# Kernel optimization log

Hardware: AMD Instinct MI355X
Metric: run time of the kernel (lower is better)

## Reference

```python
import jax, jax.numpy as jnp
import numpy as np

EMBED_DIM = 2048
NUM_HEADS = 16
HEAD_DIM = EMBED_DIM // NUM_HEADS
BASE = 10000.0


def rotate_half(x):
    half = x.shape[-1] // 2
    x1, x2 = x[..., :half], x[..., half:]
    return jnp.concatenate([-x2, x1], axis=-1)


def apply_rope(x, base=BASE):
    # x: [B, H, S, Dh]
    S, Dh = x.shape[-2], x.shape[-1]
    inv_freq = 1.0 / (base ** (jnp.arange(0, Dh, 2, dtype=jnp.float32) / Dh))
    t = jnp.arange(S, dtype=jnp.float32)
    freqs = jnp.einsum('i,j->ij', t, inv_freq)          # [S, Dh/2]
    emb = jnp.concatenate([freqs, freqs], axis=-1)      # [S, Dh]
    return x * jnp.cos(emb) + rotate_half(x) * jnp.sin(emb)


def setup_inputs() -> dict:
    key = jax.random.key(0)
    ks = jax.random.split(key, 9)
    B, S, D = 2, 2048, EMBED_DIM
    xavier = lambda k, shape: jax.random.uniform(
        k, shape, jnp.float32, -1.0, 1.0) * float(np.sqrt(6.0 / (shape[0] + shape[1])))
    return {
        'x': jax.random.normal(ks[0], (B, S, D), jnp.float32),
        'q_w': xavier(ks[1], (D, D)),
        'k_w': xavier(ks[2], (D, D)),
        'v_w': xavier(ks[3], (D, D)),
        'q_b': jnp.zeros((D,), jnp.float32),
        'k_b': jnp.zeros((D,), jnp.float32),
        'v_b': jnp.zeros((D,), jnp.float32),
        'out_w': xavier(ks[4], (D, D)),
        'out_b': jnp.zeros((D,), jnp.float32),
    }


def reference(x, q_w, k_w, v_w, q_b, k_b, v_b, out_w, out_b):
    B, S, D = x.shape
    H, Dh = NUM_HEADS, HEAD_DIM
    scaling = Dh ** -0.5
    # F.linear(x, W, b) = x @ W.T + b
    q = (x @ q_w.T + q_b).reshape(B, S, H, Dh).transpose(0, 2, 1, 3)
    k = (x @ k_w.T + k_b).reshape(B, S, H, Dh).transpose(0, 2, 1, 3)
    v = (x @ v_w.T + v_b).reshape(B, S, H, Dh).transpose(0, 2, 1, 3)
    q = apply_rope(q)
    k = apply_rope(k)
    attn = jnp.einsum('bhqd,bhkd->bhqk', q, k) * scaling
    probs = jax.nn.softmax(attn, axis=-1)
    out = jnp.einsum('bhqk,bhkd->bhqd', probs, v)
    out = out.transpose(0, 2, 1, 3).reshape(B, S, D)
    return out @ out_w.T + out_b
```

## Files before the change

### kernel.cpp

```cpp
#include <hip/hip_runtime.h>
#include <stdint.h>

typedef __bf16 bf16;
typedef __bf16 bf16x4 __attribute__((ext_vector_type(4)));
typedef __bf16 bf16x8 __attribute__((ext_vector_type(8)));
typedef float f32x4 __attribute__((ext_vector_type(4)));

#define DM 2048
#define MM 4096
#define MFMA16(a, b, c) __builtin_amdgcn_mfma_f32_16x16x32_bf16(a, b, c, 0, 0, 0)

__device__ __forceinline__ void gload_lds16(const void* g, void* l) {
  __builtin_amdgcn_global_load_lds((const __attribute__((address_space(1))) uint32_t*)g,
                                   (__attribute__((address_space(3))) uint32_t*)l, 16, 0, 0);
}

__global__ __launch_bounds__(256) void cvt_f32_bf16(
    const float* __restrict__ s0, const float* __restrict__ s1,
    const float* __restrict__ s2, const float* __restrict__ s3,
    const float* __restrict__ s4,
    bf16* __restrict__ d0, bf16* __restrict__ d1, bf16* __restrict__ d2,
    bf16* __restrict__ d3, bf16* __restrict__ d4)
{
  const size_t i4 = (size_t)(blockIdx.x * 256 + threadIdx.x) * 4;
  const float* s; bf16* d; size_t off;
  if      (i4 <  8388608u) { s = s0; d = d0; off = i4;             }
  else if (i4 < 12582912u) { s = s1; d = d1; off = i4 -  8388608u; }
  else if (i4 < 16777216u) { s = s2; d = d2; off = i4 - 12582912u; }
  else if (i4 < 20971520u) { s = s3; d = d3; off = i4 - 16777216u; }
  else                     { s = s4; d = d4; off = i4 - 20971520u; }
  const float4 v = *(const float4*)(s + off);
  bf16x4 o = { (bf16)v.x, (bf16)v.y, (bf16)v.z, (bf16)v.w };
  *(bf16x4*)(d + off) = o;
}

__global__ __launch_bounds__(256) void gemm_qkv(
    const bf16* __restrict__ A,
    const bf16* __restrict__ Wq, const bf16* __restrict__ Wk, const bf16* __restrict__ Wv,
    const float* __restrict__ qb, const float* __restrict__ kb, const float* __restrict__ vb,
    bf16* __restrict__ Cq, bf16* __restrict__ Ck, bf16* __restrict__ Cv)
{
  const int bz = blockIdx.z;
  const bf16*  W    = (bz == 0) ? Wq : (bz == 1) ? Wk : Wv;
  const float* bias = (bz == 0) ? qb : (bz == 1) ? kb : vb;

  __shared__ __align__(16) bf16 As[128 * 32];
  __shared__ __align__(16) bf16 Bs[128 * 32];
  const int t = threadIdx.x;
  const int wave = t >> 6, lane = t & 63;
  const int quad = lane >> 4, c16 = lane & 15;
  const int wr = wave >> 1, wc = wave & 1;
  const int m0 = blockIdx.y * 128, n0 = blockIdx.x * 128;

  f32x4 acc[4][4] = {};

  const int rowA = t >> 2;
  const int colA = (t & 3) * 8;
  const bf16* gA = A + (size_t)(m0 + rowA) * DM + colA;
  const bf16* gB = W + (size_t)(n0 + rowA) * DM + colA;
  bf16* lA = As + wave * 512;
  bf16* lB = Bs + wave * 512;

  for (int k0 = 0; k0 < DM; k0 += 32) {
    gload_lds16(gA, lA);
    gload_lds16(gA + (size_t)64 * DM, lA + 2048);
    gload_lds16(gB, lB);
    gload_lds16(gB + (size_t)64 * DM, lB + 2048);
    gA += 32; gB += 32;
    __syncthreads();

    bf16x8 af[4], bfr[4];
#pragma unroll
    for (int i = 0; i < 4; ++i)
      af[i] = *(const bf16x8*)&As[(wr * 64 + i * 16 + c16) * 32 + quad * 8];
#pragma unroll
    for (int j = 0; j < 4; ++j)
      bfr[j] = *(const bf16x8*)&Bs[(wc * 64 + j * 16 + c16) * 32 + quad * 8];
#pragma unroll
    for (int i = 0; i < 4; ++i)
#pragma unroll
      for (int j = 0; j < 4; ++j)
        acc[i][j] = MFMA16(af[i], bfr[j], acc[i][j]);
    __syncthreads();
  }

  if (bz != 2) {
    bf16* C = (bz == 0) ? Cq : Ck;
#pragma unroll
    for (int j = 0; j < 4; ++j) {
      const int col = n0 + wc * 64 + j * 16 + c16;
      const float bv = bias[col];
#pragma unroll
      for (int i = 0; i < 4; ++i) {
        const int row = m0 + wr * 64 + i * 16 + quad * 4;
#pragma unroll
        for (int r = 0; r < 4; ++r)
          C[(size_t)(row + r) * DM + col] = (bf16)(acc[i][j][r] + bv);
      }
    }
  } else {
    const int h = blockIdx.x;
#pragma unroll
    for (int j = 0; j < 4; ++j) {
      const int d = wc * 64 + j * 16 + c16;
      const float bv = bias[n0 + d];
#pragma unroll
      for (int i = 0; i < 4; ++i) {
        const int row = m0 + wr * 64 + i * 16 + quad * 4;
        const int b = row >> 11, s = row & 2047;
        bf16x4 o;
#pragma unroll
        for (int r = 0; r < 4; ++r) o[r] = (bf16)(acc[i][j][r] + bv);
        *(bf16x4*)&Cv[((size_t)((b * 16 + h) * 128 + d)) * 2048 + s] = o;
      }
    }
  }
}

__global__ __launch_bounds__(256) void gemm_bias_f32(
    const bf16* __restrict__ A, const bf16* __restrict__ W,
    const float* __restrict__ bias, float* __restrict__ C)
{
  __shared__ __align__(16) bf16 As[128 * 32];
  __shared__ __align__(16) bf16 Bs[128 * 32];
  const int t = threadIdx.x;
  const int wave = t >> 6, lane = t & 63;
  const int quad = lane >> 4, c16 = lane & 15;
  const int wr = wave >> 1, wc = wave & 1;
  const int m0 = blockIdx.y * 128, n0 = blockIdx.x * 128;

  f32x4 acc[4][4] = {};
  const int rowA = t >> 2;
  const int colA = (t & 3) * 8;
  const bf16* gA = A + (size_t)(m0 + rowA) * DM + colA;
  const bf16* gB = W + (size_t)(n0 + rowA) * DM + colA;
  bf16* lA = As + wave * 512;
  bf16* lB = Bs + wave * 512;

  for (int k0 = 0; k0 < DM; k0 += 32) {
    gload_lds16(gA, lA);
    gload_lds16(gA + (size_t)64 * DM, lA + 2048);
    gload_lds16(gB, lB);
    gload_lds16(gB + (size_t)64 * DM, lB + 2048);
    gA += 32; gB += 32;
    __syncthreads();

    bf16x8 af[4], bfr[4];
#pragma unroll
    for (int i = 0; i < 4; ++i)
      af[i] = *(const bf16x8*)&As[(wr * 64 + i * 16 + c16) * 32 + quad * 8];
#pragma unroll
    for (int j = 0; j < 4; ++j)
      bfr[j] = *(const bf16x8*)&Bs[(wc * 64 + j * 16 + c16) * 32 + quad * 8];
#pragma unroll
    for (int i = 0; i < 4; ++i)
#pragma unroll
      for (int j = 0; j < 4; ++j)
        acc[i][j] = MFMA16(af[i], bfr[j], acc[i][j]);
    __syncthreads();
  }

#pragma unroll
  for (int j = 0; j < 4; ++j) {
    const int col = n0 + wc * 64 + j * 16 + c16;
    const float bv = bias[col];
#pragma unroll
    for (int i = 0; i < 4; ++i) {
      const int row = m0 + wr * 64 + i * 16 + quad * 4;
#pragma unroll
      for (int r = 0; r < 4; ++r)
        C[(size_t)(row + r) * DM + col] = acc[i][j][r] + bv;
    }
  }
}

__global__ __launch_bounds__(256) void rope_scale(bf16* __restrict__ Q, bf16* __restrict__ K)
{
  const int idx = blockIdx.x * 256 + threadIdx.x;
  const int i = idx & 63;
  const int h = (idx >> 6) & 15;
  const int s = (idx >> 10) & 2047;
  const int b = idx >> 21;
  const size_t base = ((size_t)(b * 2048 + s)) * 2048 + (size_t)h * 128;
  const float inv_freq = __expf((float)i * -0.14391156514261228f);
  float sn, cs;
  __sincosf((float)s * inv_freq, &sn, &cs);
  const float scale = 0.08838834764831845f * 1.4426950408889634f;
  const float q1 = (float)Q[base + i], q2 = (float)Q[base + i + 64];
  Q[base + i]      = (bf16)((q1 * cs - q2 * sn) * scale);
  Q[base + i + 64] = (bf16)((q2 * cs + q1 * sn) * scale);
  const float k1 = (float)K[base + i], k2 = (float)K[base + i + 64];
  K[base + i]      = (bf16)(k1 * cs - k2 * sn);
  K[base + i + 64] = (bf16)(k2 * cs + k1 * sn);
}

__global__ __launch_bounds__(256, 2) void attn(
    const bf16* __restrict__ Q, const bf16* __restrict__ K,
    const bf16* __restrict__ Vt, bf16* __restrict__ O)
{
  __shared__ __align__(16) bf16 Ks[4][64][32];
  __shared__ __align__(16) bf16 Vs[2][128][32];
  __shared__ __align__(16) bf16 Ps[4][2][16][88];
  const int t = threadIdx.x;
  const int wave = t >> 6, lane = t & 63;
  const int quad = lane >> 4, c16 = lane & 15;
  const int bh = blockIdx.y, b = bh >> 4, h = bh & 15;
  const int q0 = blockIdx.x * 128;

  bf16x8 qf[2][4];
#pragma unroll
  for (int g = 0; g < 2; ++g) {
    const bf16* qrow = Q + (size_t)(b * 2048 + q0 + wave * 32 + g * 16 + c16) * 2048
                         + (size_t)h * 128 + quad * 8;
#pragma unroll
    for (int ks = 0; ks < 4; ++ks) qf[g][ks] = *(const bf16x8*)(qrow + ks * 32);
  }

  float l_i[2] = {0.f, 0.f};
  f32x4 o_acc[2][8] = {};

  const bf16* Kg = K + (size_t)(b * 2048) * 2048 + (size_t)h * 128;
  const bf16* Vg = Vt + (size_t)bh * 128 * 2048;

  for (int kt = 0; kt < 32; ++kt) {
    const int kt0 = kt * 64;
#pragma unroll
    for (int rr = 0; rr < 4; ++rr) {
      const int s = rr * 256 + t;
      const int ks = s >> 8, krow = (s >> 2) & 63, c8 = s & 3;
      gload_lds16(Kg + (size_t)(kt0 + krow) * 2048 + ks * 32 + c8 * 8,
                  (bf16*)Ks + (size_t)(rr * 256 + wave * 64) * 8);
    }
#pragma unroll
    for (int rr = 0; rr < 4; ++rr) {
      const int s = rr * 256 + t;
      const int kc = s >> 9, d = (s >> 2) & 127, c8 = s & 3;
      gload_lds16(Vg + (size_t)d * 2048 + kt0 + kc * 32 + c8 * 8,
                  (bf16*)Vs + (size_t)(rr * 256 + wave * 64) * 8);
    }
    __syncthreads();

    f32x4 st[2][4] = {};
#pragma unroll
    for (int ks = 0; ks < 4; ++ks)
#pragma unroll
      for (int nt = 0; nt < 4; ++nt) {
        bf16x8 kf = *(const bf16x8*)&Ks[ks][nt * 16 + c16][quad * 8];
        st[0][nt] = MFMA16(kf, qf[0][ks], st[0][nt]);
        st[1][nt] = MFMA16(kf, qf[1][ks], st[1][nt]);
      }

#pragma unroll
    for (int g = 0; g < 2; ++g) {
      float ps = 0.f;
#pragma unroll
      for (int nt = 0; nt < 4; ++nt) {
        bf16x4 pk;
#pragma unroll
        for (int r = 0; r < 4; ++r) {
          const float p = exp2f(st[g][nt][r]);
          ps += p;
          pk[r] = (bf16)p;
        }
        *(bf16x4*)&Ps[wave][g][c16][nt * 16 + quad * 4] = pk;
      }
      l_i[g] += ps;
    }

#pragma unroll
    for (int kc = 0; kc < 2; ++kc) {
      bf16x8 pf0 = *(const bf16x8*)&Ps[wave][0][c16][kc * 32 + quad * 8];
      bf16x8 pf1 = *(const bf16x8*)&Ps[wave][1][c16][kc * 32 + quad * 8];
#pragma unroll
      for (int dt = 0; dt < 8; ++dt) {
        bf16x8 vf = *(const bf16x8*)&Vs[kc][dt * 16 + c16][quad * 8];
        o_acc[0][dt] = MFMA16(vf, pf0, o_acc[0][dt]);
        o_acc[1][dt] = MFMA16(vf, pf1, o_acc[1][dt]);
      }
    }
    __syncthreads();
  }

#pragma unroll
  for (int g = 0; g < 2; ++g) {
    float l = l_i[g];
    l += __shfl_xor(l, 16, 64);
    l += __shfl_xor(l, 32, 64);
    const float invl = 1.0f / l;
    const int qrow = q0 + wave * 32 + g * 16 + c16;
    bf16* orow = O + (size_t)(b * 2048 + qrow) * 2048 + (size_t)h * 128 + quad * 4;
#pragma unroll
    for (int dt = 0; dt < 8; ++dt) {
      bf16x4 o;
#pragma unroll
      for (int r = 0; r < 4; ++r) o[r] = (bf16)(o_acc[g][dt][r] * invl);
      *(bf16x4*)(orow + dt * 16) = o;
    }
  }
}

extern "C" void kernel_launch(void* const* d_in, const int* in_sizes, int n_in,
                              void* d_out, int out_size, void* d_ws, size_t ws_size,
                              hipStream_t stream)
{
  (void)in_sizes; (void)n_in; (void)out_size; (void)ws_size;
  const float* x   = (const float*)d_in[0];
  const float* q_w = (const float*)d_in[1];
  const float* k_w = (const float*)d_in[2];
  const float* v_w = (const float*)d_in[3];
  const float* q_b = (const float*)d_in[4];
  const float* k_b = (const float*)d_in[5];
  const float* v_b = (const float*)d_in[6];
  const float* o_w = (const float*)d_in[7];
  const float* o_b = (const float*)d_in[8];

  const size_t NELEM = (size_t)MM * DM;
  const size_t WELEM = (size_t)DM * DM;
  bf16* Xb  = (bf16*)d_ws;
  bf16* Wq  = Xb + NELEM;
  bf16* Wk  = Wq + WELEM;
  bf16* Wv  = Wk + WELEM;
  bf16* Wo  = Wv + WELEM;
  bf16* Q   = Wo + WELEM;
  bf16* Kb  = Q  + NELEM;
  bf16* Vt  = Kb + NELEM;
  bf16* attnO = Xb;

  cvt_f32_bf16<<<24576, 256, 0, stream>>>(x, q_w, k_w, v_w, o_w, Xb, Wq, Wk, Wv, Wo);

  gemm_qkv<<<dim3(16, 32, 3), 256, 0, stream>>>(Xb, Wq, Wk, Wv, q_b, k_b, v_b, Q, Kb, Vt);
  rope_scale<<<16384, 256, 0, stream>>>(Q, Kb);
  attn<<<dim3(16, 32), 256, 0, stream>>>(Q, Kb, Vt, attnO);
  gemm_bias_f32<<<dim3(16, 32), 256, 0, stream>>>(attnO, Wo, o_b, (float*)d_out);
}
```

Before: 435.6 us.

## Fuse Q/K/V projections into one GEMM sharing A tile and remap blocks per XCD

The three QKV projection GEMMs become one kernel in which each block loads its A tile once and multiplies it against the Wq, Wk and Wv tiles, keeping 48 accumulator fragments. This removes the repeated A loads across the three grid z-slices. All GEMM and attention launches also move to a 1D grid that is remapped so consecutive blocks on the same XCD share N-columns or heads, for better L2 locality. The cost is much higher register pressure in the fused kernel (launch bounds of 2 blocks per CU), fewer blocks overall (512 instead of 1536), and more LDS per block.

```diff
diff --git a/kernel.cpp b/kernel.cpp
--- a/kernel.cpp
+++ b/kernel.cpp
@@ -34,83 +34,98 @@
   *(bf16x4*)(d + off) = o;
 }
 
-__global__ __launch_bounds__(256) void gemm_qkv(
+__global__ __launch_bounds__(256, 2) void gemm_qkv_fused(
     const bf16* __restrict__ A,
     const bf16* __restrict__ Wq, const bf16* __restrict__ Wk, const bf16* __restrict__ Wv,
     const float* __restrict__ qb, const float* __restrict__ kb, const float* __restrict__ vb,
     bf16* __restrict__ Cq, bf16* __restrict__ Ck, bf16* __restrict__ Cv)
 {
-  const int bz = blockIdx.z;
-  const bf16*  W    = (bz == 0) ? Wq : (bz == 1) ? Wk : Wv;
-  const float* bias = (bz == 0) ? qb : (bz == 1) ? kb : vb;
-
   __shared__ __align__(16) bf16 As[128 * 32];
-  __shared__ __align__(16) bf16 Bs[128 * 32];
+  __shared__ __align__(16) bf16 Ws[3 * 128 * 32];
+  const int id = blockIdx.x;
+  const int xcd = id & 7, jj = id >> 3;
+  const int n0 = (xcd * 2 + (jj >> 5)) * 128;
+  const int m0 = (jj & 31) * 128;
+
   const int t = threadIdx.x;
   const int wave = t >> 6, lane = t & 63;
   const int quad = lane >> 4, c16 = lane & 15;
   const int wr = wave >> 1, wc = wave & 1;
-  const int m0 = blockIdx.y * 128, n0 = blockIdx.x * 128;
-
-  f32x4 acc[4][4] = {};
+
+  f32x4 acc[3][4][4] = {};
 
   const int rowA = t >> 2;
   const int colA = (t & 3) * 8;
-  const bf16* gA = A + (size_t)(m0 + rowA) * DM + colA;
-  const bf16* gB = W + (size_t)(n0 + rowA) * DM + colA;
-  bf16* lA = As + wave * 512;
-  bf16* lB = Bs + wave * 512;
+  const bf16* gA  = A  + (size_t)(m0 + rowA) * DM + colA;
+  const bf16* gW0 = Wq + (size_t)(n0 + rowA) * DM + colA;
+  const bf16* gW1 = Wk + (size_t)(n0 + rowA) * DM + colA;
+  const bf16* gW2 = Wv + (size_t)(n0 + rowA) * DM + colA;
+  bf16* lA  = As + wave * 512;
+  bf16* lW0 = Ws + wave * 512;
+  bf16* lW1 = Ws + 4096 + wave * 512;
+  bf16* lW2 = Ws + 8192 + wave * 512;
 
   for (int k0 = 0; k0 < DM; k0 += 32) {
-    gload_lds16(gA, lA);
-    gload_lds16(gA + (size_t)64 * DM, lA + 2048);
-    gload_lds16(gB, lB);
-    gload_lds16(gB + (size_t)64 * DM, lB + 2048);
-    gA += 32; gB += 32;
-    __syncthreads();
-
-    bf16x8 af[4], bfr[4];
+    gload_lds16(gA,  lA);
+    gload_lds16(gA  + (size_t)64 * DM, lA  + 2048);
+    gload_lds16(gW0, lW0);
+    gload_lds16(gW0 + (size_t)64 * DM, lW0 + 2048);
+    gload_lds16(gW1, lW1);
+    gload_lds16(gW1 + (size_t)64 * DM, lW1 + 2048);
+    gload_lds16(gW2, lW2);
+    gload_lds16(gW2 + (size_t)64 * DM, lW2 + 2048);
+    gA += 32; gW0 += 32; gW1 += 32; gW2 += 32;
+    __syncthreads();
+
+    bf16x8 af[4];
 #pragma unroll
     for (int i = 0; i < 4; ++i)
       af[i] = *(const bf16x8*)&As[(wr * 64 + i * 16 + c16) * 32 + quad * 8];
 #pragma unroll
-    for (int j = 0; j < 4; ++j)
-      bfr[j] = *(const bf16x8*)&Bs[(wc * 64 + j * 16 + c16) * 32 + quad * 8];
-#pragma unroll
-    for (int i = 0; i < 4; ++i)
-#pragma unroll
-      for (int j = 0; j < 4; ++j)
-        acc[i][j] = MFMA16(af[i], bfr[j], acc[i][j]);
-    __syncthreads();
-  }
-
-  if (bz != 2) {
-    bf16* C = (bz == 0) ? Cq : Ck;
-#pragma unroll
-    for (int j = 0; j < 4; ++j) {
-      const int col = n0 + wc * 64 + j * 16 + c16;
+    for (int z = 0; z < 3; ++z) {
+      bf16x8 bfr[4];
+#pragma unroll
+      for (int jx = 0; jx < 4; ++jx)
+        bfr[jx] = *(const bf16x8*)&Ws[z * 4096 + (wc * 64 + jx * 16 + c16) * 32 + quad * 8];
+#pragma unroll
+      for (int i = 0; i < 4; ++i)
+#pragma unroll
+        for (int jx = 0; jx < 4; ++jx)
+          acc[z][i][jx] = MFMA16(af[i], bfr[jx], acc[z][i][jx]);
+    }
+    __syncthreads();
+  }
+
+#pragma unroll
+  for (int z = 0; z < 2; ++z) {
+    bf16* C = (z == 0) ? Cq : Ck;
+    const float* bias = (z == 0) ? qb : kb;
+#pragma unroll
+    for (int jx = 0; jx < 4; ++jx) {
+      const int col = n0 + wc * 64 + jx * 16 + c16;
       const float bv = bias[col];
 #pragma unroll
       for (int i = 0; i < 4; ++i) {
         const int row = m0 + wr * 64 + i * 16 + quad * 4;
 #pragma unroll
         for (int r = 0; r < 4; ++r)
-          C[(size_t)(row + r) * DM + col] = (bf16)(acc[i][j][r] + bv);
-      }
-    }
-  } else {
-    const int h = blockIdx.x;
-#pragma unroll
-    for (int j = 0; j < 4; ++j) {
-      const int d = wc * 64 + j * 16 + c16;
-      const float bv = bias[n0 + d];
+          C[(size_t)(row + r) * DM + col] = (bf16)(acc[z][i][jx][r] + bv);
+      }
+    }
+  }
+  {
+    const int h = n0 >> 7;
+#pragma unroll
+    for (int jx = 0; jx < 4; ++jx) {
+      const int d = wc * 64 + jx * 16 + c16;
+      const float bv = vb[n0 + d];
 #pragma unroll
       for (int i = 0; i < 4; ++i) {
         const int row = m0 + wr * 64 + i * 16 + quad * 4;
         const int b = row >> 11, s = row & 2047;
         bf16x4 o;
 #pragma unroll
-        for (int r = 0; r < 4; ++r) o[r] = (bf16)(acc[i][j][r] + bv);
+        for (int r = 0; r < 4; ++r) o[r] = (bf16)(acc[2][i][jx][r] + bv);
         *(bf16x4*)&Cv[((size_t)((b * 16 + h) * 128 + d)) * 2048 + s] = o;
       }
     }
@@ -123,11 +138,15 @@
 {
   __shared__ __align__(16) bf16 As[128 * 32];
   __shared__ __align__(16) bf16 Bs[128 * 32];
+  const int id = blockIdx.x;
+  const int xcd = id & 7, jj = id >> 3;
+  const int n0 = (xcd * 2 + (jj >> 5)) * 128;
+  const int m0 = (jj & 31) * 128;
+
   const int t = threadIdx.x;
   const int wave = t >> 6, lane = t & 63;
   const int quad = lane >> 4, c16 = lane & 15;
   const int wr = wave >> 1, wc = wave & 1;
-  const int m0 = blockIdx.y * 128, n0 = blockIdx.x * 128;
 
   f32x4 acc[4][4] = {};
   const int rowA = t >> 2;
@@ -150,26 +169,26 @@
     for (int i = 0; i < 4; ++i)
       af[i] = *(const bf16x8*)&As[(wr * 64 + i * 16 + c16) * 32 + quad * 8];
 #pragma unroll
-    for (int j = 0; j < 4; ++j)
-      bfr[j] = *(const bf16x8*)&Bs[(wc * 64 + j * 16 + c16) * 32 + quad * 8];
+    for (int jx = 0; jx < 4; ++jx)
+      bfr[jx] = *(const bf16x8*)&Bs[(wc * 64 + jx * 16 + c16) * 32 + quad * 8];
 #pragma unroll
     for (int i = 0; i < 4; ++i)
 #pragma unroll
-      for (int j = 0; j < 4; ++j)
-        acc[i][j] = MFMA16(af[i], bfr[j], acc[i][j]);
-    __syncthreads();
-  }
-
-#pragma unroll
-  for (int j = 0; j < 4; ++j) {
-    const int col = n0 + wc * 64 + j * 16 + c16;
+      for (int jx = 0; jx < 4; ++jx)
+        acc[i][jx] = MFMA16(af[i], bfr[jx], acc[i][jx]);
+    __syncthreads();
+  }
+
+#pragma unroll
+  for (int jx = 0; jx < 4; ++jx) {
+    const int col = n0 + wc * 64 + jx * 16 + c16;
     const float bv = bias[col];
 #pragma unroll
     for (int i = 0; i < 4; ++i) {
       const int row = m0 + wr * 64 + i * 16 + quad * 4;
 #pragma unroll
       for (int r = 0; r < 4; ++r)
-        C[(size_t)(row + r) * DM + col] = acc[i][j][r] + bv;
+        C[(size_t)(row + r) * DM + col] = acc[i][jx][r] + bv;
     }
   }
 }
@@ -204,8 +223,11 @@
   const int t = threadIdx.x;
   const int wave = t >> 6, lane = t & 63;
   const int quad = lane >> 4, c16 = lane & 15;
-  const int bh = blockIdx.y, b = bh >> 4, h = bh & 15;
-  const int q0 = blockIdx.x * 128;
+  const int id = blockIdx.x;
+  const int xcd = id & 7, jj = id >> 3;
+  const int bh = xcd * 4 + (jj >> 4);
+  const int q0 = (jj & 15) * 128;
+  const int b = bh >> 4, h = bh & 15;
 
   bf16x8 qf[2][4];
 #pragma unroll
@@ -328,8 +350,8 @@
 
   cvt_f32_bf16<<<24576, 256, 0, stream>>>(x, q_w, k_w, v_w, o_w, Xb, Wq, Wk, Wv, Wo);
 
-  gemm_qkv<<<dim3(16, 32, 3), 256, 0, stream>>>(Xb, Wq, Wk, Wv, q_b, k_b, v_b, Q, Kb, Vt);
+  gemm_qkv_fused<<<512, 256, 0, stream>>>(Xb, Wq, Wk, Wv, q_b, k_b, v_b, Q, Kb, Vt);
   rope_scale<<<16384, 256, 0, stream>>>(Q, Kb);
-  attn<<<dim3(16, 32), 256, 0, stream>>>(Q, Kb, Vt, attnO);
-  gemm_bias_f32<<<dim3(16, 32), 256, 0, stream>>>(attnO, Wo, o_b, (float*)d_out);
-}
+  attn<<<512, 256, 0, stream>>>(Q, Kb, Vt, attnO);
+  gemm_bias_f32<<<512, 256, 0, stream>>>(attnO, Wo, o_b, (float*)d_out);
+}
```

After: 410.8 us. 5.7% less time.
